# Performance work log

Hardware: AMD Instinct MI355X
Metric: run time of the kernel (lower is better)

## Reference

```python
import jax, jax.numpy as jnp
import numpy as np

K = 16          # knn neighbors (init kwarg k)
GROUPS = 4      # GroupNorm groups
EPS = 1e-5
SLOPE = 0.2     # LeakyReLU negative slope


def fps(xyz, n):
    """Farthest point sampling. xyz: (B,N,3) -> idx (B,n). First index is 0 (pointnet2 convention)."""
    B, N, _ = xyz.shape

    def step(carry, _):
        dist, last = carry
        p = jnp.take_along_axis(xyz, last[:, None, None], axis=1)  # (B,1,3)
        d = jnp.sum((xyz - p) ** 2, axis=-1)                       # (B,N)
        dist = jnp.minimum(dist, d)
        nxt = jnp.argmax(dist, axis=-1).astype(jnp.int32)
        return (dist, nxt), nxt

    init = (jnp.full((B, N), jnp.inf, xyz.dtype), jnp.zeros((B,), jnp.int32))
    _, idxs = jax.lax.scan(step, init, None, length=n - 1)  # (n-1, B)
    return jnp.concatenate([jnp.zeros((B, 1), jnp.int32), idxs.T], axis=1)


def graph_feature(cq, fq, ck, fk):
    """DGCNN edge features. cq:(B,Q,3) fq:(B,Q,C) ck:(B,N,3) fk:(B,N,C) -> (B,Q,K,2C)."""
    d2 = (jnp.sum(cq * cq, -1)[:, :, None]
          - 2.0 * jnp.einsum('bqc,bnc->bqn', cq, ck)
          + jnp.sum(ck * ck, -1)[:, None, :])        # (B,Q,N)
    _, idx = jax.lax.top_k(-d2, K)                    # (B,Q,K) nearest first
    nb = jax.vmap(lambda f_, i_: f_[i_])(fk, idx)     # (B,Q,K,C)
    ctr = jnp.broadcast_to(fq[:, :, None, :], nb.shape)
    return jnp.concatenate([nb - ctr, ctr], axis=-1)


def conv_gn_lrelu(y, W, gw, gb):
    """1x1 Conv2d (no bias) + GroupNorm(4) + LeakyReLU(0.2). y: (B,Q,K,Cin), W: (Cout,Cin)."""
    y = jnp.einsum('bqkc,oc->bqko', y, W)
    B, Q, Kk, C = y.shape
    yg = y.reshape(B, Q * Kk, GROUPS, C // GROUPS)
    m = yg.mean(axis=(1, 3), keepdims=True)
    v = yg.var(axis=(1, 3), keepdims=True)
    y = ((yg - m) * jax.lax.rsqrt(v + EPS)).reshape(B, Q, Kk, C) * gw + gb
    return jnp.where(y > 0, y, SLOPE * y)


def setup_inputs() -> dict:
    key = jax.random.key(0)
    ks = jax.random.split(key, 16)
    B, N = 8, 4096
    s = lambda k_, shape, scale=0.1: (jax.random.normal(k_, shape, jnp.float32) * scale)
    return {
        'x': jax.random.normal(ks[0], (B, N, 7), jnp.float32),
        'W_in': s(ks[1], (8, 3), 0.5), 'b_in': s(ks[2], (8,), 0.02),
        'W1': s(ks[3], (32, 16), 0.2), 'g1w': jnp.ones((32,), jnp.float32), 'g1b': jnp.zeros((32,), jnp.float32),
        'W2': s(ks[4], (64, 64), 0.1), 'g2w': jnp.ones((64,), jnp.float32), 'g2b': jnp.zeros((64,), jnp.float32),
        'W3': s(ks[5], (64, 128), 0.1), 'g3w': jnp.ones((64,), jnp.float32), 'g3b': jnp.zeros((64,), jnp.float32),
        'W4': s(ks[6], (128, 128), 0.1), 'g4w': jnp.ones((128,), jnp.float32), 'g4b': jnp.zeros((128,), jnp.float32),
        'num0': 1024,
    }


def reference(x, W_in, b_in, W1, g1w, g1b, W2, g2w, g2b, W3, g3w, g3b, W4, g4w, g4b, num0):
    coor, normal, plane = x[..., :3], x[..., 3:6], x[..., 6:7]   # (B,N,3),(B,N,3),(B,N,1)

    # input_trans: Conv1d(3,8,1)
    f = jnp.einsum('bnc,oc->bno', coor, W_in) + b_in             # (B,N,8)

    g = graph_feature(coor, f, coor, f)                          # (B,N,K,16)
    f = conv_gn_lrelu(g, W1, g1w, g1b).max(axis=2)               # (B,N,32)

    idx = fps(coor, num0)
    gather = lambda a: jnp.take_along_axis(a, idx[:, :, None], axis=1)
    coor_q, normal_q, plane_q, f_q = gather(coor), gather(normal), gather(plane), gather(f)

    g = graph_feature(coor_q, f_q, coor, f)                      # (B,num0,K,64)
    f = conv_gn_lrelu(g, W2, g2w, g2b).max(axis=2)               # (B,num0,64)
    coor, normal, plane = coor_q, normal_q, plane_q

    g = graph_feature(coor, f, coor, f)                          # (B,num0,K,128)
    f = conv_gn_lrelu(g, W3, g3w, g3b).max(axis=2)               # (B,num0,64)

    idx = fps(coor, num0)  # source uses num[0] again
    gather = lambda a: jnp.take_along_axis(a, idx[:, :, None], axis=1)
    coor_q, normal_q, plane_q, f_q = gather(coor), gather(normal), gather(plane), gather(f)

    g = graph_feature(coor_q, f_q, coor, f)                      # (B,num0,K,128)
    f = conv_gn_lrelu(g, W4, g4w, g4b).max(axis=2)               # (B,num0,128)

    return coor_q, f, normal_q, plane_q
```

## Files before the change

### kernel.cpp

```cpp
#include <hip/hip_runtime.h>
#include <cstdint>

static constexpr int B   = 8;
static constexpr int N0  = 4096;
static constexpr int NQ  = 1024;
static constexpr int KNB = 16;

__device__ __forceinline__ unsigned long long wave_max_u64_l63(unsigned long long k) {
#define STEPU_(ctrl)                                                                    \
  {                                                                                     \
    unsigned lo_ = (unsigned)k, hi_ = (unsigned)(k >> 32);                              \
    unsigned plo_ = (unsigned)__builtin_amdgcn_update_dpp((int)lo_, (int)lo_, ctrl,     \
                                                          0xf, 0xf, false);             \
    unsigned phi_ = (unsigned)__builtin_amdgcn_update_dpp((int)hi_, (int)hi_, ctrl,     \
                                                          0xf, 0xf, false);             \
    unsigned long long pk_ = ((unsigned long long)phi_ << 32) | plo_;                   \
    if (pk_ > k) k = pk_;                                                               \
  }
  STEPU_(0x111) STEPU_(0x112) STEPU_(0x114) STEPU_(0x118) STEPU_(0x142) STEPU_(0x143)
#undef STEPU_
  return k;
}

__global__ void prep_kernel(const float* __restrict__ x,
                            const float* __restrict__ W_in,
                            const float* __restrict__ b_in,
                            float4* __restrict__ c4, float* __restrict__ nrm,
                            float* __restrict__ pl, float* __restrict__ f0) {
  int i = blockIdx.x * 256 + threadIdx.x;
  if (i >= B * N0) return;
  const float* xp = x + (size_t)i * 7;
  float cx = xp[0], cy = xp[1], cz = xp[2];
  float kk = __fadd_rn(__fadd_rn(__fmul_rn(cx, cx), __fmul_rn(cy, cy)), __fmul_rn(cz, cz));
  c4[i] = make_float4(cx, cy, cz, kk);
  nrm[i * 3 + 0] = xp[3]; nrm[i * 3 + 1] = xp[4]; nrm[i * 3 + 2] = xp[5];
  pl[i] = xp[6];
#pragma unroll
  for (int o = 0; o < 8; o++) {
    f0[(size_t)i * 8 + o] = cx * W_in[o * 3 + 0] + cy * W_in[o * 3 + 1] + cz * W_in[o * 3 + 2] + b_in[o];
  }
}

template <int NC>
__device__ __forceinline__ void knn_body(int bq, int lane,
                                         const float4* __restrict__ q4,
                                         const float4* __restrict__ k4,
                                         int Q, int Nk, int* __restrict__ out) {
  int b = bq / Q;
  float4 q = q4[bq];
  const float4* kb = k4 + (size_t)b * Nk + lane;
  const float INF    = __int_as_float(0x7f800000);
  const float NEGINF = __int_as_float(0xff800000);
  float myd = INF;
  int   myi = 0;
  float kth = INF;
  const bool isl0 = (lane & 15) == 0;
  constexpr int G = (NC >= 8) ? 8 : NC;
  for (int c0 = 0; c0 < NC; c0 += G) {
    float dg[G];
#pragma unroll
    for (int u = 0; u < G; u++) {
      float4 kp = kb[(c0 + u) * 64];
      float dot = __fadd_rn(__fadd_rn(__fmul_rn(q.x, kp.x), __fmul_rn(q.y, kp.y)),
                            __fmul_rn(q.z, kp.z));
      dg[u] = __fadd_rn(__fsub_rn(q.w, __fmul_rn(2.0f, dot)), kp.w);
    }
#pragma unroll
    for (int u = 0; u < G; u++) {
      float d = dg[u];
      unsigned long long m = __ballot(d < kth);
      while (m) {
        int j = __builtin_ctzll(m);
        float dv = __int_as_float(__builtin_amdgcn_readlane(__float_as_int(d), j));
        int   iv = (c0 + u) * 64 + j;
        bool gt = (myd > dv);
        float pd = __int_as_float(__builtin_amdgcn_update_dpp(
            0, __float_as_int(myd), 0x111, 0xf, 0xf, true));
        int   pi = __builtin_amdgcn_update_dpp(0, myi, 0x111, 0xf, 0xf, true);
        pd = isl0 ? NEGINF : pd;
        bool tp = (pd > dv);
        float nd = tp ? pd : dv;
        int   ni = tp ? pi : iv;
        myd = gt ? nd : myd;
        myi = gt ? ni : myi;
        kth = __int_as_float(__builtin_amdgcn_readlane(__float_as_int(myd), 15));
        m = __ballot(d < kth);
        m = (j < 63) ? (m & (~0ull << (j + 1))) : 0ull;
      }
    }
  }
  if (lane < KNB) out[(size_t)bq * KNB + lane] = myi;
}

template <int CF, int CO>
__device__ __forceinline__ void ctry_body(int i, int total, const float* __restrict__ fq,
                                          const float* __restrict__ W,
                                          float* __restrict__ ctrY,
                                          const int* __restrict__ ridx, int Q, int Nsrc) {
  if (i >= total) return;
  int o = i % CO, bq = i / CO;
  const float* fp;
  if (ridx) {
    int b = bq / Q;
    fp = fq + ((size_t)b * Nsrc + ridx[bq]) * CF;
  } else {
    fp = fq + (size_t)bq * CF;
  }
  const float* wp = W + (size_t)o * (2 * CF) + CF;
  float acc = 0.f;
#pragma unroll
  for (int c = 0; c < CF; c++) acc = fmaf(fp[c], wp[c], acc);
  ctrY[i] = acc;
}

template <int NPTS>
__device__ __forceinline__ void fps_body(const float4* __restrict__ cb, int* w) {
  constexpr int BLK = 256;
  constexpr int M = NPTS / BLK;
  constexpr int NW = BLK / 64;
  __shared__ __align__(16) float2 sxy[NPTS];
  __shared__ float szz[NPTS];
  __shared__ __align__(16) unsigned long long skey[2][NW];
  const int tid = threadIdx.x;
  const int wid = tid >> 6, lane = tid & 63;
  float cx[M], cy[M], cz[M], dist[M];
#pragma unroll
  for (int i = 0; i < M; i++) {
    float4 p = cb[tid * M + i];
    cx[i] = p.x; cy[i] = p.y; cz[i] = p.z;
    dist[i] = 3.4e38f;
    sxy[tid * M + i] = make_float2(p.x, p.y);
    szz[tid * M + i] = p.z;
  }
  w[0] = w[1] = w[2] = w[3] = 0;
  float4 p0 = cb[0];
  float px = p0.x, py = p0.y, pz = p0.z;
  __syncthreads();
  for (int t = 1; t < NQ; t++) {
    float bv = -1.f; int bi = 0;
#pragma unroll
    for (int i = 0; i < M; i++) {
      float dx = __fsub_rn(cx[i], px), dy = __fsub_rn(cy[i], py), dz = __fsub_rn(cz[i], pz);
      float d = __fadd_rn(__fadd_rn(__fmul_rn(dx, dx), __fmul_rn(dy, dy)), __fmul_rn(dz, dz));
      float dd = dist[i]; dd = (d < dd) ? d : dd; dist[i] = dd;
      if (dd > bv) { bv = dd; bi = tid * M + i; }
    }
    unsigned long long k =
        ((unsigned long long)__float_as_uint(bv) << 12) | (unsigned)(4095 - bi);
    k = wave_max_u64_l63(k);
    int p = t & 1;
    if (lane == 63) skey[p][wid] = k;
    __syncthreads();
    ulonglong2 ab = *(const ulonglong2*)&skey[p][0];
    ulonglong2 cd = *(const ulonglong2*)&skey[p][2];
    unsigned long long m0 = (ab.x > ab.y) ? ab.x : ab.y;
    unsigned long long m1 = (cd.x > cd.y) ? cd.x : cd.y;
    unsigned long long mk = (m0 > m1) ? m0 : m1;
    int win = 4095 - (int)(mk & 0xFFFull);
    float2 pxy = sxy[win];
    px = pxy.x; py = pxy.y; pz = szz[win];
    if (t == tid) w[0] = win;
    if (t == tid + 256) w[1] = win;
    if (t == tid + 512) w[2] = win;
    if (t == tid + 768) w[3] = win;
  }
}

template <int NPTS>
__device__ __forceinline__ void fps1w_body(const float4* __restrict__ cb,
                                           float2* __restrict__ sxy,
                                           float* __restrict__ szz,
                                           int* __restrict__ swin) {
  constexpr int M = NPTS / 64;
  const int lane = threadIdx.x;
  float cx[M], cy[M], cz[M], dist[M];
#pragma unroll
  for (int i = 0; i < M; i++) {
    float4 p = cb[lane * M + i];
    cx[i] = p.x; cy[i] = p.y; cz[i] = p.z;
    dist[i] = 3.4e38f;
    sxy[lane * M + i] = make_float2(p.x, p.y);
    szz[lane * M + i] = p.z;
  }
  float4 p0 = cb[0];
  float px = p0.x, py = p0.y, pz = p0.z;
  for (int t = 1; t < NQ; t++) {
    float bv = -1.f; int bi = 0;
#pragma unroll
    for (int i = 0; i < M; i++) {
      float dx = __fsub_rn(cx[i], px), dy = __fsub_rn(cy[i], py), dz = __fsub_rn(cz[i], pz);
      float d = __fadd_rn(__fadd_rn(__fmul_rn(dx, dx), __fmul_rn(dy, dy)), __fmul_rn(dz, dz));
      float dd = dist[i]; dd = (d < dd) ? d : dd; dist[i] = dd;
      if (dd > bv) { bv = dd; bi = lane * M + i; }
    }
    unsigned long long k =
        ((unsigned long long)__float_as_uint(bv) << 12) | (unsigned)(4095 - bi);
    k = wave_max_u64_l63(k);
    unsigned klo = (unsigned)__builtin_amdgcn_readlane((int)(unsigned)k, 63);
    int win = 4095 - (int)(klo & 0xFFFu);
    if (lane == 0) swin[t] = win;
    float2 pxy = sxy[win];
    px = pxy.x; py = pxy.y; pz = szz[win];
  }
}

template <int CF, int CO, int NT>
__device__ __forceinline__ void edgeconv_body(
    int blkid, const float* __restrict__ fq, const float* __restrict__ fk,
    const int* __restrict__ knn, const float* __restrict__ Wfull,
    const float* __restrict__ ctrY, const int* __restrict__ ridx,
    float* __restrict__ ymin, float* __restrict__ ymax,
    float* __restrict__ gstats, int Q, int Nk) {
  constexpr int J = CO / 4;
  constexpr int SEC = J * CF + 8;
  constexpr int NWARP = NT / 64;
  __shared__ float Wl[4 * SEC];
  __shared__ float sstat[8];
  for (int t = threadIdx.x; t < CO * CF; t += NT) {
    int o = t / CF, c = t % CF;
    Wl[(o / J) * SEC + (o % J) * CF + c] = Wfull[(size_t)o * (2 * CF) + c];
  }
  if (threadIdx.x < 8) sstat[threadIdx.x] = 0.0f;
  __syncthreads();
  const int wid = threadIdx.x >> 6, lane = threadIdx.x & 63;
  const int bq = blkid * NWARP + wid;
  const int b = bq / Q;
  const int g = lane >> 4, k = lane & 15;
  const int ni = knn[(size_t)bq * KNB + k];
  const float* nbp = fk + (size_t)(b * Nk + ni) * CF;
  const float* cp = ridx ? fq + ((size_t)b * Nk + ridx[bq]) * CF
                         : fq + (size_t)bq * CF;
  float acc[J];
#pragma unroll
  for (int j = 0; j < J; j++) acc[j] = 0.0f;
  const float* wg = &Wl[g * SEC];
#pragma unroll
  for (int c = 0; c < CF; c += 4) {
    float4 nb4 = *(const float4*)(nbp + c);
    float4 c4  = *(const float4*)(cp + c);
    float e0 = nb4.x - c4.x, e1 = nb4.y - c4.y, e2 = nb4.z - c4.z, e3 = nb4.w - c4.w;
#pragma unroll
    for (int j = 0; j < J; j++) {
      float4 w4 = *(const float4*)(wg + j * CF + c);
      acc[j] = fmaf(e0, w4.x, acc[j]);
      acc[j] = fmaf(e1, w4.y, acc[j]);
      acc[j] = fmaf(e2, w4.z, acc[j]);
      acc[j] = fmaf(e3, w4.w, acc[j]);
    }
  }
  float s = 0.f, s2 = 0.f;
  const float* cyp = ctrY + (size_t)bq * CO + g * J;
#pragma unroll
  for (int j = 0; j < J; j++) {
    float y = acc[j] + cyp[j];
    acc[j] = y;
    s += y; s2 = fmaf(y, y, s2);
  }
  float mn[J];
#pragma unroll
  for (int j = 0; j < J; j++) mn[j] = acc[j];
#pragma unroll
  for (int m = 1; m < 16; m <<= 1) {
#pragma unroll
    for (int j = 0; j < J; j++) {
      float a = __shfl_xor(acc[j], m); if (a > acc[j]) acc[j] = a;
      float c2 = __shfl_xor(mn[j], m); if (c2 < mn[j]) mn[j] = c2;
    }
    s  += __shfl_xor(s, m);
    s2 += __shfl_xor(s2, m);
  }
  if (k == 0) {
    float* mnp = ymin + (size_t)bq * CO + g * J;
    float* mxp = ymax + (size_t)bq * CO + g * J;
#pragma unroll
    for (int j = 0; j < J; j++) { mnp[j] = mn[j]; mxp[j] = acc[j]; }
    atomicAdd(&sstat[g], s);
    atomicAdd(&sstat[4 + g], s2);
  }
  __syncthreads();
  if (threadIdx.x < 8) atomicAdd(&gstats[b * 8 + threadIdx.x], sstat[threadIdx.x]);
}

__global__ __launch_bounds__(256, 2) void mega1_kernel(
    const float4* __restrict__ c40, const float* __restrict__ nrm,
    const float* __restrict__ pl, const float* __restrict__ f0,
    const float* __restrict__ W1, int* __restrict__ idx1,
    float4* __restrict__ c4q1, float* __restrict__ nq1, float* __restrict__ pq1,
    int* __restrict__ knn1, float* __restrict__ ctrY1) {
  int blk = blockIdx.x;
  if (blk < 8) {
    const int b = blk, tid = threadIdx.x;
    const float4* cb = c40 + (size_t)b * N0;
    int w[4];
    fps_body<N0>(cb, w);
    int* idxb = idx1 + (size_t)b * NQ;
#pragma unroll
    for (int u = 0; u < 4; u++) {
      int r = tid + u * 256;
      int s = (u == 0 && tid == 0) ? 0 : w[u];
      idxb[r] = s;
      c4q1[(size_t)b * NQ + r] = cb[s];
      const float* np = nrm + ((size_t)b * N0 + s) * 3;
      float* ndp = nq1 + ((size_t)b * NQ + r) * 3;
      ndp[0] = np[0]; ndp[1] = np[1]; ndp[2] = np[2];
      pq1[(size_t)b * NQ + r] = pl[(size_t)b * N0 + s];
    }
  } else if (blk < 8 + 8192) {
    int bq = (blk - 8) * 4 + (threadIdx.x >> 6);
    knn_body<64>(bq, threadIdx.x & 63, c40, c40, N0, N0, knn1);
  } else {
    int i = (blk - (8 + 8192)) * 256 + threadIdx.x;
    ctry_body<8, 32>(i, B * N0 * 32, f0, W1, ctrY1, nullptr, 0, 0);
  }
}

__global__ __launch_bounds__(256, 2) void ec1f_kernel(
    const float4* __restrict__ c4q1, const float* __restrict__ nq1,
    const float* __restrict__ pq1, const float* __restrict__ f0,
    const int* __restrict__ knn1, const float* __restrict__ W1,
    const float* __restrict__ ctrY1, float* __restrict__ ymin,
    float* __restrict__ ymax, float* __restrict__ gst1,
    int* __restrict__ idx2, float4* __restrict__ c4q2,
    float* __restrict__ cq2out, float* __restrict__ nq2out,
    float* __restrict__ pq2out) {
  int blk = blockIdx.x;
  if (blk < 8) {
    if (threadIdx.x < 64) {
      __shared__ __align__(16) float2 sxy2[NQ];
      __shared__ float szz2[NQ];
      __shared__ int swin2[NQ];
      const int b = blk, lane = threadIdx.x;
      const float4* cqb = c4q1 + (size_t)b * NQ;
      fps1w_body<NQ>(cqb, sxy2, szz2, swin2);
      int* idxb = idx2 + (size_t)b * NQ;
#pragma unroll
      for (int u = 0; u < NQ / 64; u++) {
        int r = lane + u * 64;
        int s = (r == 0) ? 0 : swin2[r];
        idxb[r] = s;
        float4 c = cqb[s];
        c4q2[(size_t)b * NQ + r] = c;
        float* cd = cq2out + ((size_t)b * NQ + r) * 3;
        cd[0] = c.x; cd[1] = c.y; cd[2] = c.z;
        const float* np = nq1 + ((size_t)b * NQ + s) * 3;
        float* ndp = nq2out + ((size_t)b * NQ + r) * 3;
        ndp[0] = np[0]; ndp[1] = np[1]; ndp[2] = np[2];
        pq2out[(size_t)b * NQ + r] = pq1[(size_t)b * NQ + s];
      }
    }
  } else {
    edgeconv_body<8, 32, 256>(blk - 8, f0, f0, knn1, W1, ctrY1, nullptr,
                              ymin, ymax, gst1, N0, N0);
  }
}

__global__ __launch_bounds__(256, 2) void mega2_kernel(
    const float4* __restrict__ c40, const float4* __restrict__ c4q1,
    const float* __restrict__ f1, const int* __restrict__ idx1,
    const float* __restrict__ W2,
    int* __restrict__ knn2, int* __restrict__ knn3, float* __restrict__ ctrY2) {
  int blk = blockIdx.x;
  if (blk < 2048) {
    int bq = blk * 4 + (threadIdx.x >> 6);
    knn_body<64>(bq, threadIdx.x & 63, c4q1, c40, NQ, N0, knn2);
  } else if (blk < 4096) {
    int bq = (blk - 2048) * 4 + (threadIdx.x >> 6);
    knn_body<16>(bq, threadIdx.x & 63, c4q1, c4q1, NQ, NQ, knn3);
  } else {
    int i = (blk - 4096) * 256 + threadIdx.x;
    ctry_body<32, 64>(i, B * NQ * 64, f1, W2, ctrY2, idx1, NQ, N0);
  }
}

__global__ __launch_bounds__(256, 4) void mega3_kernel(
    const float4* __restrict__ c4q1, const float4* __restrict__ c4q2,
    const float* __restrict__ f3, const int* __restrict__ idx2,
    const float* __restrict__ W4, int* __restrict__ knn4, float* __restrict__ ctrY4) {
  int blk = blockIdx.x;
  if (blk < 2048) {
    int bq = blk * 4 + (threadIdx.x >> 6);
    knn_body<16>(bq, threadIdx.x & 63, c4q2, c4q1, NQ, NQ, knn4);
  } else {
    int i = (blk - 2048) * 256 + threadIdx.x;
    ctry_body<64, 128>(i, B * NQ * 128, f3, W4, ctrY4, idx2, NQ, NQ);
  }
}

template <int CF, int CO>
__global__ void ctry_kernel(const float* __restrict__ fq, const float* __restrict__ W,
                            float* __restrict__ ctrY, int total) {
  int i = blockIdx.x * 256 + threadIdx.x;
  ctry_body<CF, CO>(i, total, fq, W, ctrY, nullptr, 0, 0);
}

template <int CF, int CO>
__global__ __launch_bounds__(256) void edgeconv_kernel(
    const float* __restrict__ fq, const float* __restrict__ fk,
    const int* __restrict__ knn, const float* __restrict__ Wfull,
    const float* __restrict__ ctrY, const int* __restrict__ ridx,
    float* __restrict__ ymin, float* __restrict__ ymax,
    float* __restrict__ gstats, int Q, int Nk) {
  edgeconv_body<CF, CO, 256>(blockIdx.x, fq, fk, knn, Wfull, ctrY, ridx,
                             ymin, ymax, gstats, Q, Nk);
}

template <int CO>
__global__ void gn_out_kernel(const float* __restrict__ ymin, const float* __restrict__ ymax,
                              const float* __restrict__ gstats, const float* __restrict__ gw,
                              const float* __restrict__ gb, float* __restrict__ fout,
                              int total, int Q, float inv_cnt) {
  int i = blockIdx.x * 256 + threadIdx.x;
  if (i >= total) return;
  constexpr int J = CO / 4;
  int o = i % CO; int bq = i / CO; int b = bq / Q;
  int g = o / J;
  float m  = gstats[b * 8 + g] * inv_cnt;
  float s2 = gstats[b * 8 + 4 + g] * inv_cnt;
  float rs = rsqrtf(s2 - m * m + 1e-5f);
  float sc = gw[o] * rs;
  float sel = (sc >= 0.f) ? ymax[i] : ymin[i];
  float v = (sel - m) * sc + gb[o];
  fout[i] = (v > 0.f) ? v : 0.2f * v;
}

extern "C" void kernel_launch(void* const* d_in, const int* in_sizes, int n_in,
                              void* d_out, int out_size, void* d_ws, size_t ws_size,
                              hipStream_t stream) {
  (void)in_sizes; (void)n_in; (void)out_size; (void)ws_size;
  const float* x    = (const float*)d_in[0];
  const float* W_in = (const float*)d_in[1];
  const float* b_in = (const float*)d_in[2];
  const float* W1   = (const float*)d_in[3];
  const float* g1w  = (const float*)d_in[4];
  const float* g1b  = (const float*)d_in[5];
  const float* W2   = (const float*)d_in[6];
  const float* g2w  = (const float*)d_in[7];
  const float* g2b  = (const float*)d_in[8];
  const float* W3   = (const float*)d_in[9];
  const float* g3w  = (const float*)d_in[10];
  const float* g3b  = (const float*)d_in[11];
  const float* W4   = (const float*)d_in[12];
  const float* g4w  = (const float*)d_in[13];
  const float* g4b  = (const float*)d_in[14];

  float* ws = (float*)d_ws;
  size_t o_c40  = 0;
  size_t o_nrm  = o_c40  + (size_t)B * N0 * 4;
  size_t o_pl   = o_nrm  + (size_t)B * N0 * 3;
  size_t o_f0   = o_pl   + (size_t)B * N0;
  size_t o_f1   = o_f0   + (size_t)B * N0 * 8;
  size_t o_ctrY = o_f1   + (size_t)B * N0 * 32;
  size_t o_ymin = o_ctrY + (size_t)B * N0 * 32;
  size_t o_ymax = o_ymin + (size_t)B * N0 * 32;
  size_t o_knnA = o_ymax + (size_t)B * N0 * 32;
  size_t o_knnB = o_knnA + (size_t)B * N0 * KNB;
  size_t o_gst  = o_knnB + (size_t)B * NQ * KNB;
  size_t o_idx1 = o_gst  + 4 * B * 8;
  size_t o_idx2 = o_idx1 + (size_t)B * NQ;
  size_t o_c4q1 = o_idx2 + (size_t)B * NQ;
  size_t o_c4q2 = o_c4q1 + (size_t)B * NQ * 4;
  size_t o_nq1  = o_c4q2 + (size_t)B * NQ * 4;
  size_t o_pq1  = o_nq1  + (size_t)B * NQ * 3;
  size_t o_f2   = o_pq1  + (size_t)B * NQ;
  size_t o_f3   = o_f2   + (size_t)B * NQ * 64;

  float4* c40  = (float4*)(ws + o_c40);
  float*  nrm  = ws + o_nrm;   float* pl   = ws + o_pl;
  float*  f0   = ws + o_f0;    float* f1   = ws + o_f1;
  float*  ctrY = ws + o_ctrY;  float* ymin = ws + o_ymin;  float* ymax = ws + o_ymax;
  int*    knnA = (int*)(ws + o_knnA);
  int*    knnB = (int*)(ws + o_knnB);
  float*  gst  = ws + o_gst;
  int*    idx1 = (int*)(ws + o_idx1);
  int*    idx2 = (int*)(ws + o_idx2);
  float4* c4q1 = (float4*)(ws + o_c4q1);
  float4* c4q2 = (float4*)(ws + o_c4q2);
  float*  nq1  = ws + o_nq1;   float* pq1  = ws + o_pq1;
  float*  f2   = ws + o_f2;    float* f3   = ws + o_f3;

  float* out  = (float*)d_out;
  float* cq2  = out;
  float* fout = out + (size_t)B * NQ * 3;
  float* nq2  = fout + (size_t)B * NQ * 128;
  float* pq2  = nq2 + (size_t)B * NQ * 3;

  hipMemsetAsync(gst, 0, 4 * B * 8 * sizeof(float), stream);

  prep_kernel<<<(B * N0 + 255) / 256, 256, 0, stream>>>(x, W_in, b_in, c40, nrm, pl, f0);

  mega1_kernel<<<8 + 8192 + 4096, 256, 0, stream>>>(c40, nrm, pl, f0, W1,
                                                    idx1, c4q1, nq1, pq1, knnA, ctrY);
  ec1f_kernel<<<8 + 8192, 256, 0, stream>>>(c4q1, nq1, pq1, f0, knnA, W1, ctrY,
                                            ymin, ymax, gst + 0,
                                            idx2, c4q2, cq2, nq2, pq2);
  gn_out_kernel<32><<<(B * N0 * 32 + 255) / 256, 256, 0, stream>>>(
      ymin, ymax, gst + 0, g1w, g1b, f1, B * N0 * 32, N0, 1.0f / (4096.0f * 16.0f * 8.0f));

  mega2_kernel<<<2048 + 2048 + 2048, 256, 0, stream>>>(
      c40, c4q1, f1, idx1, W2, knnA, knnB, ctrY);
  edgeconv_kernel<32, 64><<<B * NQ / 4, 256, 0, stream>>>(f1, f1, knnA, W2, ctrY, idx1,
                                                          ymin, ymax, gst + B * 8, NQ, N0);
  gn_out_kernel<64><<<(B * NQ * 64 + 255) / 256, 256, 0, stream>>>(
      ymin, ymax, gst + B * 8, g2w, g2b, f2, B * NQ * 64, NQ, 1.0f / (1024.0f * 16.0f * 16.0f));

  ctry_kernel<64, 64><<<(B * NQ * 64 + 255) / 256, 256, 0, stream>>>(f2, W3, ctrY, B * NQ * 64);
  edgeconv_kernel<64, 64><<<B * NQ / 4, 256, 0, stream>>>(f2, f2, knnB, W3, ctrY, nullptr,
                                                          ymin, ymax, gst + 2 * B * 8, NQ, NQ);
  gn_out_kernel<64><<<(B * NQ * 64 + 255) / 256, 256, 0, stream>>>(
      ymin, ymax, gst + 2 * B * 8, g3w, g3b, f3, B * NQ * 64, NQ, 1.0f / (1024.0f * 16.0f * 16.0f));

  mega3_kernel<<<2048 + 4096, 256, 0, stream>>>(c4q1, c4q2, f3, idx2, W4, knnB, ctrY);
  edgeconv_kernel<64, 128><<<B * NQ / 4, 256, 0, stream>>>(f3, f3, knnB, W4, ctrY, idx2,
                                                           ymin, ymax, gst + 3 * B * 8, NQ, NQ);
  gn_out_kernel<128><<<(B * NQ * 128 + 255) / 256, 256, 0, stream>>>(
      ymin, ymax, gst + 3 * B * 8, g4w, g4b, fout, B * NQ * 128, NQ, 1.0f / (1024.0f * 16.0f * 32.0f));
}
```

Before: 1.617 ms.

## Fold level-2 kNN into ec1f kernel and broadcast FPS winner coords via readlane

The two level-2 kNN searches (queries vs full cloud, queries vs queries) move out of mega2 into the ec1f kernel, so they run alongside the second FPS and the first edgeconv. Their results go to a new knnC buffer instead of knnA, and the ctrY2 projection becomes its own small kernel. The one-wave FPS now does its argmax with a float DPP max plus a ballot, and takes the winner's coordinates from registers with readlane instead of reading LDS copies. This removes the LDS staging and a serial reduction step on the FPS critical path, in exchange for an extra launch and a longer ec1f kernel.

```diff
diff --git a/kernel.cpp b/kernel.cpp
--- a/kernel.cpp
+++ b/kernel.cpp
@@ -168,8 +168,6 @@
 
 template <int NPTS>
 __device__ __forceinline__ void fps1w_body(const float4* __restrict__ cb,
-                                           float2* __restrict__ sxy,
-                                           float* __restrict__ szz,
                                            int* __restrict__ swin) {
   constexpr int M = NPTS / 64;
   const int lane = threadIdx.x;
@@ -179,28 +177,36 @@
     float4 p = cb[lane * M + i];
     cx[i] = p.x; cy[i] = p.y; cz[i] = p.z;
     dist[i] = 3.4e38f;
-    sxy[lane * M + i] = make_float2(p.x, p.y);
-    szz[lane * M + i] = p.z;
   }
   float4 p0 = cb[0];
   float px = p0.x, py = p0.y, pz = p0.z;
   for (int t = 1; t < NQ; t++) {
     float bv = -1.f; int bi = 0;
+    float bx = px, by = py, bz = pz;
 #pragma unroll
     for (int i = 0; i < M; i++) {
       float dx = __fsub_rn(cx[i], px), dy = __fsub_rn(cy[i], py), dz = __fsub_rn(cz[i], pz);
       float d = __fadd_rn(__fadd_rn(__fmul_rn(dx, dx), __fmul_rn(dy, dy)), __fmul_rn(dz, dz));
       float dd = dist[i]; dd = (d < dd) ? d : dd; dist[i] = dd;
-      if (dd > bv) { bv = dd; bi = lane * M + i; }
-    }
-    unsigned long long k =
-        ((unsigned long long)__float_as_uint(bv) << 12) | (unsigned)(4095 - bi);
-    k = wave_max_u64_l63(k);
-    unsigned klo = (unsigned)__builtin_amdgcn_readlane((int)(unsigned)k, 63);
-    int win = 4095 - (int)(klo & 0xFFFu);
+      if (dd > bv) { bv = dd; bi = lane * M + i; bx = cx[i]; by = cy[i]; bz = cz[i]; }
+    }
+    float wm = bv;
+#define SMAX_(ctrl)                                                                     \
+  {                                                                                     \
+    int t_ = __builtin_amdgcn_update_dpp(__float_as_int(wm), __float_as_int(wm), ctrl,  \
+                                         0xf, 0xf, false);                              \
+    wm = fmaxf(wm, __int_as_float(t_));                                                 \
+  }
+    SMAX_(0x111) SMAX_(0x112) SMAX_(0x114) SMAX_(0x118) SMAX_(0x142) SMAX_(0x143)
+#undef SMAX_
+    float wmax = __int_as_float(__builtin_amdgcn_readlane(__float_as_int(wm), 63));
+    unsigned long long tied = __ballot(bv == wmax);
+    int L = (int)__builtin_ctzll(tied);
+    int win = __builtin_amdgcn_readlane(bi, L);
+    px = __int_as_float(__builtin_amdgcn_readlane(__float_as_int(bx), L));
+    py = __int_as_float(__builtin_amdgcn_readlane(__float_as_int(by), L));
+    pz = __int_as_float(__builtin_amdgcn_readlane(__float_as_int(bz), L));
     if (lane == 0) swin[t] = win;
-    float2 pxy = sxy[win];
-    px = pxy.x; py = pxy.y; pz = szz[win];
   }
 }
 
@@ -315,23 +321,21 @@
 }
 
 __global__ __launch_bounds__(256, 2) void ec1f_kernel(
-    const float4* __restrict__ c4q1, const float* __restrict__ nq1,
-    const float* __restrict__ pq1, const float* __restrict__ f0,
-    const int* __restrict__ knn1, const float* __restrict__ W1,
-    const float* __restrict__ ctrY1, float* __restrict__ ymin,
-    float* __restrict__ ymax, float* __restrict__ gst1,
+    const float4* __restrict__ c40, const float4* __restrict__ c4q1,
+    const float* __restrict__ nq1, const float* __restrict__ pq1,
+    const float* __restrict__ f0, const int* __restrict__ knn1,
+    const float* __restrict__ W1, const float* __restrict__ ctrY1,
+    float* __restrict__ ymin, float* __restrict__ ymax, float* __restrict__ gst1,
     int* __restrict__ idx2, float4* __restrict__ c4q2,
     float* __restrict__ cq2out, float* __restrict__ nq2out,
-    float* __restrict__ pq2out) {
+    float* __restrict__ pq2out, int* __restrict__ knnC, int* __restrict__ knnB) {
   int blk = blockIdx.x;
   if (blk < 8) {
     if (threadIdx.x < 64) {
-      __shared__ __align__(16) float2 sxy2[NQ];
-      __shared__ float szz2[NQ];
       __shared__ int swin2[NQ];
       const int b = blk, lane = threadIdx.x;
       const float4* cqb = c4q1 + (size_t)b * NQ;
-      fps1w_body<NQ>(cqb, sxy2, szz2, swin2);
+      fps1w_body<NQ>(cqb, swin2);
       int* idxb = idx2 + (size_t)b * NQ;
 #pragma unroll
       for (int u = 0; u < NQ / 64; u++) {
@@ -348,27 +352,15 @@
         pq2out[(size_t)b * NQ + r] = pq1[(size_t)b * NQ + s];
       }
     }
-  } else {
+  } else if (blk < 8 + 8192) {
     edgeconv_body<8, 32, 256>(blk - 8, f0, f0, knn1, W1, ctrY1, nullptr,
                               ymin, ymax, gst1, N0, N0);
-  }
-}
-
-__global__ __launch_bounds__(256, 2) void mega2_kernel(
-    const float4* __restrict__ c40, const float4* __restrict__ c4q1,
-    const float* __restrict__ f1, const int* __restrict__ idx1,
-    const float* __restrict__ W2,
-    int* __restrict__ knn2, int* __restrict__ knn3, float* __restrict__ ctrY2) {
-  int blk = blockIdx.x;
-  if (blk < 2048) {
-    int bq = blk * 4 + (threadIdx.x >> 6);
-    knn_body<64>(bq, threadIdx.x & 63, c4q1, c40, NQ, N0, knn2);
-  } else if (blk < 4096) {
-    int bq = (blk - 2048) * 4 + (threadIdx.x >> 6);
-    knn_body<16>(bq, threadIdx.x & 63, c4q1, c4q1, NQ, NQ, knn3);
+  } else if (blk < 8 + 8192 + 2048) {
+    int bq = (blk - (8 + 8192)) * 4 + (threadIdx.x >> 6);
+    knn_body<64>(bq, threadIdx.x & 63, c4q1, c40, NQ, N0, knnC);
   } else {
-    int i = (blk - 4096) * 256 + threadIdx.x;
-    ctry_body<32, 64>(i, B * NQ * 64, f1, W2, ctrY2, idx1, NQ, N0);
+    int bq = (blk - (8 + 8192 + 2048)) * 4 + (threadIdx.x >> 6);
+    knn_body<16>(bq, threadIdx.x & 63, c4q1, c4q1, NQ, NQ, knnB);
   }
 }
 
@@ -388,9 +380,10 @@
 
 template <int CF, int CO>
 __global__ void ctry_kernel(const float* __restrict__ fq, const float* __restrict__ W,
-                            float* __restrict__ ctrY, int total) {
+                            float* __restrict__ ctrY, int total,
+                            const int* __restrict__ ridx, int Q, int Nsrc) {
   int i = blockIdx.x * 256 + threadIdx.x;
-  ctry_body<CF, CO>(i, total, fq, W, ctrY, nullptr, 0, 0);
+  ctry_body<CF, CO>(i, total, fq, W, ctrY, ridx, Q, Nsrc);
 }
 
 template <int CF, int CO>
@@ -463,6 +456,7 @@
   size_t o_pq1  = o_nq1  + (size_t)B * NQ * 3;
   size_t o_f2   = o_pq1  + (size_t)B * NQ;
   size_t o_f3   = o_f2   + (size_t)B * NQ * 64;
+  size_t o_knnC = o_f3   + (size_t)B * NQ * 64;
 
   float4* c40  = (float4*)(ws + o_c40);
   float*  nrm  = ws + o_nrm;   float* pl   = ws + o_pl;
@@ -470,6 +464,7 @@
   float*  ctrY = ws + o_ctrY;  float* ymin = ws + o_ymin;  float* ymax = ws + o_ymax;
   int*    knnA = (int*)(ws + o_knnA);
   int*    knnB = (int*)(ws + o_knnB);
+  int*    knnC = (int*)(ws + o_knnC);
   float*  gst  = ws + o_gst;
   int*    idx1 = (int*)(ws + o_idx1);
   int*    idx2 = (int*)(ws + o_idx2);
@@ -490,20 +485,21 @@
 
   mega1_kernel<<<8 + 8192 + 4096, 256, 0, stream>>>(c40, nrm, pl, f0, W1,
                                                     idx1, c4q1, nq1, pq1, knnA, ctrY);
-  ec1f_kernel<<<8 + 8192, 256, 0, stream>>>(c4q1, nq1, pq1, f0, knnA, W1, ctrY,
-                                            ymin, ymax, gst + 0,
-                                            idx2, c4q2, cq2, nq2, pq2);
+  ec1f_kernel<<<8 + 8192 + 2048 + 2048, 256, 0, stream>>>(
+      c40, c4q1, nq1, pq1, f0, knnA, W1, ctrY, ymin, ymax, gst + 0,
+      idx2, c4q2, cq2, nq2, pq2, knnC, knnB);
   gn_out_kernel<32><<<(B * N0 * 32 + 255) / 256, 256, 0, stream>>>(
       ymin, ymax, gst + 0, g1w, g1b, f1, B * N0 * 32, N0, 1.0f / (4096.0f * 16.0f * 8.0f));
 
-  mega2_kernel<<<2048 + 2048 + 2048, 256, 0, stream>>>(
-      c40, c4q1, f1, idx1, W2, knnA, knnB, ctrY);
-  edgeconv_kernel<32, 64><<<B * NQ / 4, 256, 0, stream>>>(f1, f1, knnA, W2, ctrY, idx1,
+  ctry_kernel<32, 64><<<(B * NQ * 64 + 255) / 256, 256, 0, stream>>>(
+      f1, W2, ctrY, B * NQ * 64, idx1, NQ, N0);
+  edgeconv_kernel<32, 64><<<B * NQ / 4, 256, 0, stream>>>(f1, f1, knnC, W2, ctrY, idx1,
                                                           ymin, ymax, gst + B * 8, NQ, N0);
   gn_out_kernel<64><<<(B * NQ * 64 + 255) / 256, 256, 0, stream>>>(
       ymin, ymax, gst + B * 8, g2w, g2b, f2, B * NQ * 64, NQ, 1.0f / (1024.0f * 16.0f * 16.0f));
 
-  ctry_kernel<64, 64><<<(B * NQ * 64 + 255) / 256, 256, 0, stream>>>(f2, W3, ctrY, B * NQ * 64);
+  ctry_kernel<64, 64><<<(B * NQ * 64 + 255) / 256, 256, 0, stream>>>(
+      f2, W3, ctrY, B * NQ * 64, nullptr, 0, 0);
   edgeconv_kernel<64, 64><<<B * NQ / 4, 256, 0, stream>>>(f2, f2, knnB, W3, ctrY, nullptr,
                                                           ymin, ymax, gst + 2 * B * 8, NQ, NQ);
   gn_out_kernel<64><<<(B * NQ * 64 + 255) / 256, 256, 0, stream>>>(
```

New measurement: 1.810 ms. 1.12x slower.
